# Kernel optimization log

Measured on AMD Instinct MI355X. Metric: run time of the kernel, lower is better.

The kernel has to match this reference:

```python
import jax, jax.numpy as jnp
import numpy as np

B, L, H, NH = 1, 4096, 768, 12
HD = H // NH  # 64


def setup_inputs() -> dict:
    key = jax.random.key(0)
    ks = jax.random.split(key, 10)
    inp = {
        "query": jax.random.normal(ks[0], (B, L, H), jnp.float32),
        "key": jax.random.normal(ks[1], (B, L, H), jnp.float32),
        "value": jax.random.normal(ks[2], (B, L, H), jnp.float32),
        "attention_mask": jnp.zeros((B, 1, 1, L), jnp.float32),
        # learned params (nn.Linear: y = x @ W.T + b)
        "Wq": jax.random.normal(ks[3], (H, H), jnp.float32) * 0.02,
        "bq": jnp.zeros((H,), jnp.float32),
        "Wk": jax.random.normal(ks[4], (H, H), jnp.float32) * 0.02,
        "bk": jnp.zeros((H,), jnp.float32),
        "Wv": jax.random.normal(ks[5], (H, H), jnp.float32) * 0.02,
        "bv": jnp.zeros((H,), jnp.float32),
    }
    return inp


def _split_heads(x):
    # [B, L, H] -> [B, NH, L, HD]
    b, l, _ = x.shape
    return x.reshape(b, l, NH, HD).transpose(0, 2, 1, 3)


def reference(query, key, value, attention_mask, Wq, bq, Wk, bk, Wv, bv):
    q = _split_heads(query @ Wq.T + bq)   # [B, NH, Lq, HD]
    k = _split_heads(key @ Wk.T + bk)     # [B, NH, Lk, HD]
    v = _split_heads(value @ Wv.T + bv)   # [B, NH, Lk, HD]

    scale = 1.0 / jnp.sqrt(jnp.asarray(HD, q.dtype))
    scores = jnp.einsum("bhqd,bhkd->bhqk", q, k) * scale
    scores = scores + attention_mask  # additive mask, broadcasts over heads/queries
    probs = jax.nn.softmax(scores, axis=-1)
    # dropout is identity in eval mode (reference baseline)
    ctx = jnp.einsum("bhqk,bhkd->bhqd", probs, v)  # [B, NH, Lq, HD]
    out = ctx.transpose(0, 2, 1, 3).reshape(query.shape[0], query.shape[1], H)
    return out
```

## Files before the change

### kernel.cpp

```cpp
#include <hip/hip_runtime.h>
#include <math.h>

#define LSEQ 4096
#define HDIM 768
#define NHEAD 12

using v4f    = __attribute__((ext_vector_type(4))) float;
using short8 = __attribute__((ext_vector_type(8))) short;
using u32x4  = __attribute__((ext_vector_type(4))) unsigned int;

#if __has_builtin(__builtin_amdgcn_exp2f)
#define EXP2F(x) __builtin_amdgcn_exp2f(x)
#else
#define EXP2F(x) exp2f(x)
#endif

#define GLOAD_LDS16(g, l)                                                  \
  __builtin_amdgcn_global_load_lds(                                       \
      (const __attribute__((address_space(1))) unsigned int*)(g),         \
      (__attribute__((address_space(3))) unsigned int*)(l), 16, 0, 0)

__device__ __forceinline__ unsigned short f2bf(float f) {
  union { float f; unsigned u; } v; v.f = f;
  unsigned r = v.u + 0x7fffu + ((v.u >> 16) & 1u);
  return (unsigned short)(r >> 16);
}

__device__ __forceinline__ short8 cvt8(u32x4 a, u32x4 b) {
  short8 r;
#pragma unroll
  for (int i = 0; i < 4; ++i) {
    unsigned u = a[i];
    r[i] = (short)((u + 0x7fffu + ((u >> 16) & 1u)) >> 16);
  }
#pragma unroll
  for (int i = 0; i < 4; ++i) {
    unsigned u = b[i];
    r[4 + i] = (short)((u + 0x7fffu + ((u >> 16) & 1u)) >> 16);
  }
  return r;
}

__global__ __launch_bounds__(256, 2) void proj_gemm(
    const float* __restrict__ Xq, const float* __restrict__ Xk,
    const float* __restrict__ Xv,
    const float* __restrict__ Wq, const float* __restrict__ Wk,
    const float* __restrict__ Wv,
    const float* __restrict__ bq, const float* __restrict__ bk,
    const float* __restrict__ bv,
    unsigned short* __restrict__ dst_base)
{
  __shared__ __align__(16) unsigned short a_lds[128 * 32];
  __shared__ __align__(16) unsigned short b_lds[128 * 32];
  __shared__ __align__(16) unsigned short c_lds[64 * 136];

  const int id = blockIdx.x;
  const int xcd = id & 7, local = id >> 3;
  const int grp = local / 6, bnIdx = local % 6;
  const int G = grp * 8 + xcd;
  const int z = G >> 5;
  const int bm = (G & 31) * 128, bn = bnIdx * 128;

  const float* X = (z == 0) ? Xq : ((z == 1) ? Xk : Xv);
  const float* W = (z == 0) ? Wq : ((z == 1) ? Wk : Wv);
  const float* bias = (z == 0) ? bq : ((z == 1) ? bk : bv);
  unsigned short* dst = dst_base + (size_t)z * NHEAD * LSEQ * 64;

  const int tid = threadIdx.x;
  const int wave = tid >> 6, lane = tid & 63;
  const int quad = lane >> 4, l16 = lane & 15;
  const int wm = (wave >> 1) * 64, wn = (wave & 1) * 64;

  v4f acc[4][4];
  for (int i = 0; i < 4; ++i)
    for (int j = 0; j < 4; ++j)
      acc[i][j] = (v4f){0.f, 0.f, 0.f, 0.f};

  const int row_s = tid >> 2;
  const int c8_s = (tid & 3) * 8;

  const float* xrow[2]; const float* wrow[2];
#pragma unroll
  for (int s = 0; s < 2; ++s) {
    xrow[s] = X + (size_t)(bm + row_s + 64 * s) * HDIM + c8_s;
    wrow[s] = W + (size_t)(bn + row_s + 64 * s) * HDIM + c8_s;
  }

  u32x4 pa[2][2], pb[2][2];
#pragma unroll
  for (int s = 0; s < 2; ++s) {
    pa[s][0] = *(const u32x4*)(xrow[s]);     pa[s][1] = *(const u32x4*)(xrow[s] + 4);
    pb[s][0] = *(const u32x4*)(wrow[s]);     pb[s][1] = *(const u32x4*)(wrow[s] + 4);
  }

  for (int k0 = 0; k0 < HDIM; k0 += 32) {
    __syncthreads();
#pragma unroll
    for (int s = 0; s < 2; ++s) {
      *(short8*)&a_lds[(row_s + 64 * s) * 32 + c8_s] = cvt8(pa[s][0], pa[s][1]);
      *(short8*)&b_lds[(row_s + 64 * s) * 32 + c8_s] = cvt8(pb[s][0], pb[s][1]);
    }
    __syncthreads();

    if (k0 + 32 < HDIM) {
#pragma unroll
      for (int s = 0; s < 2; ++s) {
        pa[s][0] = *(const u32x4*)(xrow[s] + k0 + 32);
        pa[s][1] = *(const u32x4*)(xrow[s] + k0 + 36);
        pb[s][0] = *(const u32x4*)(wrow[s] + k0 + 32);
        pb[s][1] = *(const u32x4*)(wrow[s] + k0 + 36);
      }
    }

    short8 af[4], bfr[4];
    for (int i = 0; i < 4; ++i)
      af[i] = *(const short8*)&a_lds[(wm + i * 16 + l16) * 32 + quad * 8];
    for (int j = 0; j < 4; ++j)
      bfr[j] = *(const short8*)&b_lds[(wn + j * 16 + l16) * 32 + quad * 8];
    if (z == 2) {
      for (int i = 0; i < 4; ++i)
        for (int j = 0; j < 4; ++j)
          acc[i][j] = __builtin_amdgcn_mfma_f32_16x16x32_bf16(bfr[j], af[i], acc[i][j], 0, 0, 0);
    } else {
      for (int i = 0; i < 4; ++i)
        for (int j = 0; j < 4; ++j)
          acc[i][j] = __builtin_amdgcn_mfma_f32_16x16x32_bf16(af[i], bfr[j], acc[i][j], 0, 0, 0);
    }
  }

  for (int p = 0; p < 2; ++p) {
    __syncthreads();
    if (z == 2) {
      if ((wave & 1) == p) {
        for (int j = 0; j < 4; ++j)
          for (int r = 0; r < 4; ++r) {
            float bvv = bias[bn + wn + j * 16 + quad * 4 + r];
            int row = j * 16 + quad * 4 + r;
            for (int i = 0; i < 4; ++i)
              c_lds[row * 136 + wm + i * 16 + l16] = f2bf(acc[i][j][r] + bvv);
          }
      }
    } else {
      if ((wave >> 1) == p) {
        for (int j = 0; j < 4; ++j) {
          float bvv = bias[bn + wn + j * 16 + l16];
          for (int i = 0; i < 4; ++i)
            for (int r = 0; r < 4; ++r)
              c_lds[(i * 16 + quad * 4 + r) * 136 + wn + j * 16 + l16] =
                  f2bf(acc[i][j][r] + bvv);
        }
      }
    }
    __syncthreads();
    int row = tid >> 2, c = tid & 3;
    const unsigned short* srow = &c_lds[row * 136 + c * 32];
    if (z == 2) {
      int n = bn + p * 64 + row;
      int hh = n >> 6, d = n & 63;
      unsigned short* drow = dst + ((size_t)hh * 64 + d) * LSEQ + bm + c * 32;
      for (int q8 = 0; q8 < 4; ++q8)
        *(u32x4*)(drow + q8 * 8) = *(const u32x4*)(srow + q8 * 8);
    } else {
      int m = bm + p * 64 + row;
      int nbase = bn + c * 32;
      int hh = nbase >> 6, d = nbase & 63;
      unsigned short* drow = dst + ((size_t)hh * LSEQ + m) * 64 + d;
      for (int q8 = 0; q8 < 4; ++q8)
        *(u32x4*)(drow + q8 * 8) = *(const u32x4*)(srow + q8 * 8);
    }
  }
}

__global__ __launch_bounds__(256, 4) void attn(
    const unsigned short* __restrict__ Q, const unsigned short* __restrict__ K,
    const unsigned short* __restrict__ Vt, const float* __restrict__ mask,
    float* __restrict__ out)
{
  __shared__ __align__(16) unsigned short k_lds[2][64 * 64];
  __shared__ __align__(16) unsigned short vt_lds[2][64 * 64];
  __shared__ __align__(16) unsigned short p_lds[4][16 * 64];

  const int h = blockIdx.y;
  const int qt = blockIdx.x;
  const int tid = threadIdx.x;
  const int wave = tid >> 6, lane = tid & 63;
  const int quad = lane >> 4, l16 = lane & 15;

  const unsigned short* Qh  = Q  + (size_t)h * LSEQ * 64;
  const unsigned short* Kh  = K  + (size_t)h * LSEQ * 64;
  const unsigned short* Vth = Vt + (size_t)h * 64 * LSEQ;

  const unsigned short* ksrc[2]; const unsigned short* vsrc[2];
  unsigned short* kdst[2]; unsigned short* vdst[2];
#pragma unroll
  for (int s = 0; s < 2; ++s) {
    int seg = wave * 2 + s;
    int rl = lane >> 3, cc = (lane & 7) ^ rl;
    ksrc[s] = Kh + (size_t)(seg * 8 + rl) * 64 + cc * 8;
    vsrc[s] = Vth + (size_t)(seg * 8 + rl) * LSEQ + cc * 8;
    kdst[s] = &k_lds[0][seg * 512];
    vdst[s] = &vt_lds[0][seg * 512];
  }

  int pswzW[4];
#pragma unroll
  for (int r = 0; r < 4; ++r) {
    int row = quad * 4 + r;
    pswzW[r] = (row ^ (row >> 2)) & 7;
  }
  const int pswzR = (l16 ^ (l16 >> 2)) & 7;
  const int phi = l16 >> 3, plo = l16 & 7;

  const int qrow = qt * 64 + wave * 16;
  short8 qf[2];
  for (int c = 0; c < 2; ++c)
    qf[c] = *(const short8*)(Qh + (size_t)(qrow + l16) * 64 + c * 32 + quad * 8);

  short8 ones;
#pragma unroll
  for (int i = 0; i < 8; ++i) ones[i] = (short)0x3F80;

  v4f acc_o[4];
  for (int j = 0; j < 4; ++j) acc_o[j] = (v4f){0.f, 0.f, 0.f, 0.f};
  v4f acc_l = (v4f){0.f, 0.f, 0.f, 0.f};

#pragma unroll
  for (int s = 0; s < 2; ++s) { GLOAD_LDS16(ksrc[s], kdst[s]); GLOAD_LDS16(vsrc[s], vdst[s]); }

  for (int kt = 0; kt < 64; ++kt) {
    const int key0 = kt * 64;
    const int buf = kt & 1, nbuf = (kt + 1) & 1;

    __syncthreads();

    if (kt < 63) {
      size_t ko = (size_t)(key0 + 64) * 64;
#pragma unroll
      for (int s = 0; s < 2; ++s) {
        GLOAD_LDS16(ksrc[s] + ko, kdst[s] + nbuf * 4096);
        GLOAD_LDS16(vsrc[s] + (key0 + 64), vdst[s] + nbuf * 4096);
      }
    }

    float mk[4];
#pragma unroll
    for (int j = 0; j < 4; ++j) mk[j] = mask[key0 + j * 16 + l16] * 1.44269504f;

    v4f sacc[4];
#pragma unroll
    for (int j = 0; j < 4; ++j) sacc[j] = (v4f){0.f, 0.f, 0.f, 0.f};
#pragma unroll
    for (int c = 0; c < 2; ++c)
#pragma unroll
      for (int j = 0; j < 4; ++j) {
        int row = j * 16 + l16;
        short8 kf = *(const short8*)&k_lds[buf][row * 64 + (((c * 4 + quad) ^ (row & 7)) << 3)];
        sacc[j] = __builtin_amdgcn_mfma_f32_16x16x32_bf16(qf[c], kf, sacc[j], 0, 0, 0);
      }

#pragma unroll
    for (int j = 0; j < 4; ++j) {
#pragma unroll
      for (int r = 0; r < 4; ++r) {
        union { float f; unsigned u; } pu;
        pu.f = EXP2F(fmaf(sacc[j][r], 0.18033688f, mk[j]));
        p_lds[wave][(quad * 4 + r) * 64 + (((2 * j + phi) ^ pswzW[r]) << 3) + plo] =
            (unsigned short)(pu.u >> 16);
      }
    }
    short8 pf[2];
#pragma unroll
    for (int c = 0; c < 2; ++c)
      pf[c] = *(const short8*)&p_lds[wave][l16 * 64 + (((c * 4 + quad) ^ pswzR) << 3)];

#pragma unroll
    for (int kk = 0; kk < 2; ++kk) {
#pragma unroll
      for (int j = 0; j < 4; ++j) {
        int d = j * 16 + l16;
        short8 vf = *(const short8*)&vt_lds[buf][d * 64 + (((kk * 4 + quad) ^ (d & 7)) << 3)];
        acc_o[j] = __builtin_amdgcn_mfma_f32_16x16x32_bf16(pf[kk], vf, acc_o[j], 0, 0, 0);
      }
      acc_l = __builtin_amdgcn_mfma_f32_16x16x32_bf16(pf[kk], ones, acc_l, 0, 0, 0);
    }
  }

  for (int j = 0; j < 4; ++j) {
    int col = h * 64 + j * 16 + l16;
    for (int r = 0; r < 4; ++r) {
      int row = qt * 64 + wave * 16 + quad * 4 + r;
      out[(size_t)row * HDIM + col] = acc_o[j][r] / acc_l[r];
    }
  }
}

extern "C" void kernel_launch(void* const* d_in, const int* in_sizes, int n_in,
                              void* d_out, int out_size, void* d_ws, size_t ws_size,
                              hipStream_t stream) {
  const float* query = (const float*)d_in[0];
  const float* key   = (const float*)d_in[1];
  const float* value = (const float*)d_in[2];
  const float* mask  = (const float*)d_in[3];
  const float* Wq = (const float*)d_in[4];
  const float* bq = (const float*)d_in[5];
  const float* Wk = (const float*)d_in[6];
  const float* bk = (const float*)d_in[7];
  const float* Wv = (const float*)d_in[8];
  const float* bv = (const float*)d_in[9];
  float* out = (float*)d_out;

  unsigned short* Qb = (unsigned short*)d_ws;
  unsigned short* Kb = Qb + (size_t)NHEAD * LSEQ * 64;
  unsigned short* Vb = Kb + (size_t)NHEAD * LSEQ * 64;

  proj_gemm<<<576, 256, 0, stream>>>(
      query, key, value, Wq, Wk, Wv, bq, bk, bv, Qb);
  attn<<<dim3(LSEQ / 64, NHEAD), 256, 0, stream>>>(Qb, Kb, Vb, mask, out);
}
```

Before: 236.3 us.

## Split attention key tile across wave pairs with 32-row query groups and merge

```diff
diff --git a/kernel.cpp b/kernel.cpp
--- a/kernel.cpp
+++ b/kernel.cpp
@@ -171,20 +171,22 @@
   }
 }
 
-__global__ __launch_bounds__(256, 4) void attn(
+__global__ __launch_bounds__(256, 3) void attn(
     const unsigned short* __restrict__ Q, const unsigned short* __restrict__ K,
     const unsigned short* __restrict__ Vt, const float* __restrict__ mask,
     float* __restrict__ out)
 {
   __shared__ __align__(16) unsigned short k_lds[2][64 * 64];
   __shared__ __align__(16) unsigned short vt_lds[2][64 * 64];
-  __shared__ __align__(16) unsigned short p_lds[4][16 * 64];
+  __shared__ __align__(16) unsigned short p_lds[4][32 * 64];
+  __shared__ float lsum_lds[2][32];
 
   const int h = blockIdx.y;
   const int qt = blockIdx.x;
   const int tid = threadIdx.x;
   const int wave = tid >> 6, lane = tid & 63;
   const int quad = lane >> 4, l16 = lane & 15;
+  const int qg = wave & 1, kh = wave >> 1;
 
   const unsigned short* Qh  = Q  + (size_t)h * LSEQ * 64;
   const unsigned short* Kh  = K  + (size_t)h * LSEQ * 64;
@@ -202,27 +204,32 @@
     vdst[s] = &vt_lds[0][seg * 512];
   }
 
-  int pswzW[4];
-#pragma unroll
-  for (int r = 0; r < 4; ++r) {
-    int row = quad * 4 + r;
-    pswzW[r] = (row ^ (row >> 2)) & 7;
-  }
-  const int pswzR = (l16 ^ (l16 >> 2)) & 7;
-  const int phi = l16 >> 3, plo = l16 & 7;
-
-  const int qrow = qt * 64 + wave * 16;
-  short8 qf[2];
-  for (int c = 0; c < 2; ++c)
-    qf[c] = *(const short8*)(Qh + (size_t)(qrow + l16) * 64 + c * 32 + quad * 8);
+  short8 qf[2][2];
+#pragma unroll
+  for (int i = 0; i < 2; ++i)
+#pragma unroll
+    for (int c = 0; c < 2; ++c)
+      qf[i][c] = *(const short8*)(Qh + (size_t)(qt * 64 + qg * 32 + i * 16 + l16) * 64 +
+                                  c * 32 + quad * 8);
+
+  int pswzR[2];
+#pragma unroll
+  for (int i = 0; i < 2; ++i) {
+    int rr = i * 16 + l16;
+    pswzR[i] = (rr ^ (rr >> 2)) & 7;
+  }
 
   short8 ones;
 #pragma unroll
   for (int i = 0; i < 8; ++i) ones[i] = (short)0x3F80;
 
-  v4f acc_o[4];
-  for (int j = 0; j < 4; ++j) acc_o[j] = (v4f){0.f, 0.f, 0.f, 0.f};
-  v4f acc_l = (v4f){0.f, 0.f, 0.f, 0.f};
+  v4f acc_o[2][4];
+#pragma unroll
+  for (int i = 0; i < 2; ++i)
+    for (int j = 0; j < 4; ++j) acc_o[i][j] = (v4f){0.f, 0.f, 0.f, 0.f};
+  v4f acc_l[2];
+  acc_l[0] = (v4f){0.f, 0.f, 0.f, 0.f};
+  acc_l[1] = (v4f){0.f, 0.f, 0.f, 0.f};
 
 #pragma unroll
   for (int s = 0; s < 2; ++s) { GLOAD_LDS16(ksrc[s], kdst[s]); GLOAD_LDS16(vsrc[s], vdst[s]); }
@@ -242,54 +249,95 @@
       }
     }
 
-    float mk[4];
-#pragma unroll
-    for (int j = 0; j < 4; ++j) mk[j] = mask[key0 + j * 16 + l16] * 1.44269504f;
-
-    v4f sacc[4];
-#pragma unroll
-    for (int j = 0; j < 4; ++j) sacc[j] = (v4f){0.f, 0.f, 0.f, 0.f};
+    float mk[2];
+#pragma unroll
+    for (int kg = 0; kg < 2; ++kg)
+      mk[kg] = mask[key0 + kh * 32 + kg * 16 + l16] * 1.44269504f;
+
+    v4f sacc[2][2];
+#pragma unroll
+    for (int i = 0; i < 2; ++i)
+      for (int kg = 0; kg < 2; ++kg) sacc[i][kg] = (v4f){0.f, 0.f, 0.f, 0.f};
 #pragma unroll
     for (int c = 0; c < 2; ++c)
 #pragma unroll
+      for (int kg = 0; kg < 2; ++kg) {
+        int row = kh * 32 + kg * 16 + l16;
+        short8 kf = *(const short8*)&k_lds[buf][row * 64 + (((c * 4 + quad) ^ (row & 7)) << 3)];
+#pragma unroll
+        for (int i = 0; i < 2; ++i)
+          sacc[i][kg] = __builtin_amdgcn_mfma_f32_16x16x32_bf16(qf[i][c], kf, sacc[i][kg], 0, 0, 0);
+      }
+
+#pragma unroll
+    for (int i = 0; i < 2; ++i)
+#pragma unroll
+      for (int kg = 0; kg < 2; ++kg)
+#pragma unroll
+        for (int r = 0; r < 4; ++r) {
+          union { float f; unsigned u; } pu;
+          pu.f = EXP2F(fmaf(sacc[i][kg][r], 0.18033688f, mk[kg]));
+          int prow = i * 16 + quad * 4 + r;
+          int col = kg * 16 + l16;
+          int swz = (prow ^ (prow >> 2)) & 7;
+          p_lds[wave][prow * 64 + (((col >> 3) ^ swz) << 3) + (col & 7)] =
+              (unsigned short)(pu.u >> 16);
+        }
+    short8 pf[2];
+#pragma unroll
+    for (int i = 0; i < 2; ++i)
+      pf[i] = *(const short8*)&p_lds[wave][(i * 16 + l16) * 64 + (((quad ^ pswzR[i]) & 7) << 3)];
+
+    short8 vfj[4];
+#pragma unroll
+    for (int j = 0; j < 4; ++j) {
+      int d = j * 16 + l16;
+      vfj[j] = *(const short8*)&vt_lds[buf][d * 64 + (((kh * 4 + quad) ^ (d & 7)) << 3)];
+    }
+#pragma unroll
+    for (int i = 0; i < 2; ++i) {
+#pragma unroll
+      for (int j = 0; j < 4; ++j)
+        acc_o[i][j] = __builtin_amdgcn_mfma_f32_16x16x32_bf16(pf[i], vfj[j], acc_o[i][j], 0, 0, 0);
+      acc_l[i] = __builtin_amdgcn_mfma_f32_16x16x32_bf16(pf[i], ones, acc_l[i], 0, 0, 0);
+    }
+  }
+
+  __syncthreads();
+  float* merge = (float*)&p_lds[0][0];
+  if (kh == 1) {
+#pragma unroll
+    for (int i = 0; i < 2; ++i) {
+#pragma unroll
+      for (int j = 0; j < 4; ++j)
+#pragma unroll
+        for (int r = 0; r < 4; ++r)
+          merge[qg * 2048 + (i * 16 + quad * 4 + r) * 64 + j * 16 + l16] = acc_o[i][j][r];
+      if (l16 == 0)
+#pragma unroll
+        for (int r = 0; r < 4; ++r)
+          lsum_lds[qg][i * 16 + quad * 4 + r] = acc_l[i][r];
+    }
+  }
+  __syncthreads();
+  if (kh == 0) {
+#pragma unroll
+    for (int i = 0; i < 2; ++i) {
+      float den[4];
+#pragma unroll
+      for (int r = 0; r < 4; ++r)
+        den[r] = acc_l[i][r] + lsum_lds[qg][i * 16 + quad * 4 + r];
+#pragma unroll
       for (int j = 0; j < 4; ++j) {
-        int row = j * 16 + l16;
-        short8 kf = *(const short8*)&k_lds[buf][row * 64 + (((c * 4 + quad) ^ (row & 7)) << 3)];
-        sacc[j] = __builtin_amdgcn_mfma_f32_16x16x32_bf16(qf[c], kf, sacc[j], 0, 0, 0);
-      }
-
-#pragma unroll
-    for (int j = 0; j < 4; ++j) {
-#pragma unroll
-      for (int r = 0; r < 4; ++r) {
-        union { float f; unsigned u; } pu;
-        pu.f = EXP2F(fmaf(sacc[j][r], 0.18033688f, mk[j]));
-        p_lds[wave][(quad * 4 + r) * 64 + (((2 * j + phi) ^ pswzW[r]) << 3) + plo] =
-            (unsigned short)(pu.u >> 16);
-      }
-    }
-    short8 pf[2];
-#pragma unroll
-    for (int c = 0; c < 2; ++c)
-      pf[c] = *(const short8*)&p_lds[wave][l16 * 64 + (((c * 4 + quad) ^ pswzR) << 3)];
-
-#pragma unroll
-    for (int kk = 0; kk < 2; ++kk) {
-#pragma unroll
-      for (int j = 0; j < 4; ++j) {
-        int d = j * 16 + l16;
-        short8 vf = *(const short8*)&vt_lds[buf][d * 64 + (((kk * 4 + quad) ^ (d & 7)) << 3)];
-        acc_o[j] = __builtin_amdgcn_mfma_f32_16x16x32_bf16(pf[kk], vf, acc_o[j], 0, 0, 0);
-      }
-      acc_l = __builtin_amdgcn_mfma_f32_16x16x32_bf16(pf[kk], ones, acc_l, 0, 0, 0);
-    }
-  }
-
-  for (int j = 0; j < 4; ++j) {
-    int col = h * 64 + j * 16 + l16;
-    for (int r = 0; r < 4; ++r) {
-      int row = qt * 64 + wave * 16 + quad * 4 + r;
-      out[(size_t)row * HDIM + col] = acc_o[j][r] / acc_l[r];
+        int col = h * 64 + j * 16 + l16;
+#pragma unroll
+        for (int r = 0; r < 4; ++r) {
+          int row = qt * 64 + qg * 32 + i * 16 + quad * 4 + r;
+          float o = acc_o[i][j][r] +
+                    merge[qg * 2048 + (i * 16 + quad * 4 + r) * 64 + j * 16 + l16];
+          out[(size_t)row * HDIM + col] = o / den[r];
+        }
+      }
     }
   }
 }
```

After: 228.3 us. 3.4% less time.
